# Optimization experiments

Hardware: AMD Instinct MI355X
Metric: run time of the kernel (lower is better)

The kernel has to match this reference:

```python
import jax, jax.numpy as jnp
import numpy as np

IN_F = 512
OUT_F = 512
NOISE_DIM = 128
BATCH = 512
OUT_DIM = IN_F * OUT_F + OUT_F  # 262656
PRIOR_STD = 1.0
PRIOR_SCALE = 1.0
POSTERIOR_SCALE = 1.0


def setup_inputs() -> dict:
    key = jax.random.key(0)
    k1, k2, k3, k4, k5, k6 = jax.random.split(key, 6)
    x = jax.random.normal(k1, (BATCH, IN_F), dtype=jnp.float32)
    prior_x = jax.random.normal(k2, (BATCH, IN_F), dtype=jnp.float32)
    hyper_noise = jax.random.normal(k3, (BATCH, NOISE_DIM), dtype=jnp.float32)
    # hypermodel = nn.Linear(noise_dim, out_dim): kaiming-uniform-ish init approximated by uniform
    bound = 1.0 / np.sqrt(NOISE_DIM)
    hW = jax.random.uniform(k4, (OUT_DIM, NOISE_DIM), jnp.float32, -bound, bound)
    hb = jax.random.uniform(k5, (OUT_DIM,), jnp.float32, -bound, bound)
    # PriorHyperLinear: row-normalized gaussian weight scaled by prior_std (eye), zero bias (prior_mean=0)
    pW = jax.random.normal(k6, (OUT_DIM, NOISE_DIM), dtype=jnp.float32)
    pW = PRIOR_STD * pW / jnp.linalg.norm(pW, axis=1, keepdims=True)
    pb = jnp.zeros((OUT_DIM,), dtype=jnp.float32)
    return {"x": x, "prior_x": prior_x, "hyper_noise": hyper_noise,
            "hW": hW, "hb": hb, "pW": pW, "pb": pb}


def _base_forward(x, params):
    # params: [B, in*out + out] -> per-sample weight [B, in, out], bias [B, out]
    weight = params[:, : IN_F * OUT_F].reshape(-1, IN_F, OUT_F)
    bias = params[:, IN_F * OUT_F:]  # [B, out]
    # bmm(x[:,None,:], weight) + bias -> [B, out]
    return jnp.einsum("bi,bio->bo", x, weight) + bias


def reference(x, prior_x, hyper_noise, hW, hb, pW, pb):
    params = hyper_noise @ hW.T + hb  # [B, out_dim]
    out = _base_forward(x, params)
    prior_params = hyper_noise @ pW.T + pb
    prior_out = _base_forward(prior_x, prior_params)
    return out * POSTERIOR_SCALE + prior_out * PRIOR_SCALE
```

## Files before the change

kernel.cpp:

```cpp
#include <hip/hip_runtime.h>
#include <hip/hip_fp16.h>

#define BATCH 512
#define INF   512
#define OUTF  512
#define ND    128
#define WPART 262144

typedef __attribute__((ext_vector_type(8))) _Float16 half8;
typedef __attribute__((ext_vector_type(2))) _Float16 half2v;
typedef __attribute__((ext_vector_type(4))) float    f32x4;

__device__ inline half8 cvt8(float4 a, float4 b) {
  half2v h0 = __builtin_bit_cast(half2v, __builtin_amdgcn_cvt_pkrtz(a.x, a.y));
  half2v h1 = __builtin_bit_cast(half2v, __builtin_amdgcn_cvt_pkrtz(a.z, a.w));
  half2v h2 = __builtin_bit_cast(half2v, __builtin_amdgcn_cvt_pkrtz(b.x, b.y));
  half2v h3 = __builtin_bit_cast(half2v, __builtin_amdgcn_cvt_pkrtz(b.z, b.w));
  half8 r = { h0[0], h0[1], h1[0], h1[1], h2[0], h2[1], h3[0], h3[1] };
  return r;
}

__global__ void __launch_bounds__(256) transpose_kernel(
    const float* __restrict__ x, const float* __restrict__ px,
    float* __restrict__ xt) {
  __shared__ float t[32][33];
  const float* src = blockIdx.z ? px : x;
  float* dst = xt + ((size_t)blockIdx.z << 18);
  const int bi = blockIdx.x * 32, bb = blockIdx.y * 32;
  const int tx = threadIdx.x & 31, ty = threadIdx.x >> 5;
  #pragma unroll
  for (int r = 0; r < 32; r += 8)
    t[ty + r][tx] = src[(size_t)(bb + ty + r) * 512 + bi + tx];
  __syncthreads();
  #pragma unroll
  for (int r = 0; r < 32; r += 8)
    dst[(size_t)(bi + ty + r) * 512 + bb + tx] = t[tx][ty + r];
}

__global__ void __launch_bounds__(256) tail_kernel(
    const float* __restrict__ hn, const float* __restrict__ hW,
    const float* __restrict__ pW, float* __restrict__ TT) {
  const int bt = blockIdx.x & 7;
  const int bg = blockIdx.x >> 3;
  __shared__ float wsum[64][132];
  __shared__ float hs[32][132];
  {
    int r = threadIdx.x >> 2, seg = threadIdx.x & 3;
    const float4* h4 = (const float4*)(hW + (((size_t)(WPART + bt*64 + r)) << 7) + seg*32);
    const float4* p4 = (const float4*)(pW + (((size_t)(WPART + bt*64 + r)) << 7) + seg*32);
    #pragma unroll
    for (int qq = 0; qq < 8; ++qq) {
      float4 a = h4[qq], b = p4[qq];
      float* d = &wsum[r][seg*32 + qq*4];
      d[0]=a.x+b.x; d[1]=a.y+b.y; d[2]=a.z+b.z; d[3]=a.w+b.w;
    }
    int bb = threadIdx.x >> 3, ch = threadIdx.x & 7;
    const float4* hh = (const float4*)(hn + (((size_t)(bg*32 + bb)) << 7) + ch*16);
    #pragma unroll
    for (int qq = 0; qq < 4; ++qq) {
      float4 a = hh[qq];
      float* d = &hs[bb][ch*16 + qq*4];
      d[0]=a.x; d[1]=a.y; d[2]=a.z; d[3]=a.w;
    }
  }
  __syncthreads();
  const int ol = threadIdx.x & 63, b0 = (threadIdx.x >> 6) * 8;
  float a[8] = {};
  for (int n = 0; n < 128; n += 4) {
    float4 wv = *(const float4*)&wsum[ol][n];
    #pragma unroll
    for (int r = 0; r < 8; ++r) {
      float4 hv = *(const float4*)&hs[b0 + r][n];
      a[r] += hv.x*wv.x + hv.y*wv.y + hv.z*wv.z + hv.w*wv.w;
    }
  }
  #pragma unroll
  for (int r = 0; r < 8; ++r)
    TT[(((size_t)(bg*32 + b0 + r)) << 9) + bt*64 + ol] = a[r];
}

__global__ void __launch_bounds__(1024, 4) gemm_kernel(
    const float* __restrict__ xt, const float* __restrict__ hn,
    const float* __restrict__ hW, const float* __restrict__ pW,
    float* __restrict__ P, int S) {
  const int tid = threadIdx.x;
  const int lane = tid & 63, w = tid >> 6;
  const int l15 = lane & 15, j = lane >> 4;
  const int wrow0 = w << 5;

  const int n0 = blockIdx.x << 6;
  const int q  = blockIdx.y;
  const int spb  = S >> 3;
  const int half = S >> 1;
  const int part = q / half;
  const int rem  = q % half;
  const int nh   = rem / spb;
  const int irange = 512 / spb;
  const int i0   = (rem % spb) * irange;
  const int nst  = irange >> 1;
  const float* srcW = part ? pW : hW;
  const float* xtp  = xt + ((size_t)part << 18);
  const int woff = nh << 5;

  __shared__ half8 ldsW[2][512];
  __shared__ float xr[2][2][512];

  f32x4 acc[2][4] = {};

  const int o_s = tid >> 4;
  const int g_s = tid & 15;
  const int isub_s = g_s >> 3;
  const size_t colbase = (((size_t)(n0 + o_s)) << 7) + woff + ((g_s & 7) << 2);
  const int wdst = (o_s << 7) + (((((g_s >> 1)) ^ (o_s & 7)) << 4) | ((g_s & 1) << 3));

  half8 hnf[2];
  #pragma unroll
  for (int m = 0; m < 2; ++m) {
    int row = wrow0 + m * 16 + l15;
    const float4* hp = (const float4*)(hn + ((size_t)row << 7) + woff + (j << 3));
    hnf[m] = cvt8(hp[0], hp[1]);
  }

  auto loadW = [&](int ph, float4& rw) {
    int i = i0 + 2 * ph + isub_s;
    rw = *(const float4*)(srcW + ((size_t)i << 16) + colbase);
  };
  auto writeW = [&](int buf, float4 rw) {
    unsigned u0 = __builtin_bit_cast(unsigned, __builtin_amdgcn_cvt_pkrtz(rw.x, rw.y));
    unsigned u1 = __builtin_bit_cast(unsigned, __builtin_amdgcn_cvt_pkrtz(rw.z, rw.w));
    uint2 u; u.x = u0; u.y = u1;
    *(uint2*)((char*)&ldsW[buf][0] + wdst) = u;
  };
  auto stageX = [&](int buf, int ph) {
    int i = i0 + 2 * ph + (tid >> 9);
    const float* g = xtp + ((size_t)i << 9) + (tid & 511);
    __builtin_amdgcn_global_load_lds(
        (const __attribute__((address_space(1))) void*)g,
        (__attribute__((address_space(3))) void*)((char*)&xr[buf][0][0] + tid * 4),
        4, 0, 0);
  };
  auto compute = [&](int buf) {
    const char* bW = (const char*)&ldsW[buf][0];
    #pragma unroll
    for (int kk = 0; kk < 2; ++kk) {
      half8 af[2], bf[4];
      #pragma unroll
      for (int m = 0; m < 2; ++m) {
        float xv = xr[buf][kk][wrow0 + m * 16 + l15];
        _Float16 t = (_Float16)xv;
        half8 xb = { t, t, t, t, t, t, t, t };
        af[m] = hnf[m] * xb;
      }
      #pragma unroll
      for (int nn = 0; nn < 4; ++nn) {
        int byte = (((nn << 4) + l15) << 7) + (((((kk << 2) + j)) ^ (l15 & 7)) << 4);
        bf[nn] = *(const half8*)(bW + byte);
      }
      __builtin_amdgcn_s_setprio(1);
      #pragma unroll
      for (int m = 0; m < 2; ++m)
        #pragma unroll
        for (int nn = 0; nn < 4; ++nn)
          acc[m][nn] = __builtin_amdgcn_mfma_f32_16x16x32_f16(
              af[m], bf[nn], acc[m][nn], 0, 0, 0);
      __builtin_amdgcn_s_setprio(0);
    }
  };

  float4 rwA, rwB;
  asm volatile("s_waitcnt vmcnt(0)" ::: "memory");
  loadW(0, rwA);
  stageX(0, 0);
  loadW(1, rwB);
  writeW(0, rwA);

  for (int p = 0; p < nst; p += 2) {
    asm volatile("s_waitcnt vmcnt(1) lgkmcnt(0)" ::: "memory");
    __builtin_amdgcn_s_barrier();
    stageX(1, p + 1);
    if (p + 2 < nst) loadW(p + 2, rwA);
    compute(0);
    writeW(1, rwB);

    if (p + 2 < nst)
      asm volatile("s_waitcnt vmcnt(1) lgkmcnt(0)" ::: "memory");
    else
      asm volatile("s_waitcnt vmcnt(0) lgkmcnt(0)" ::: "memory");
    __builtin_amdgcn_s_barrier();
    if (p + 2 < nst) stageX(0, p + 2);
    if (p + 3 < nst) loadW(p + 3, rwB);
    compute(1);
    if (p + 2 < nst) writeW(0, rwA);
  }

  float* outp = P + ((size_t)q << 18);
  #pragma unroll
  for (int m = 0; m < 2; ++m) {
    int row = wrow0 + m * 16 + (j << 2);
    #pragma unroll
    for (int nn = 0; nn < 4; ++nn) {
      int col = n0 + (nn << 4) + l15;
      float* op = outp + (size_t)row * OUTF + col;
      op[0]    = acc[m][nn][0];
      op[512]  = acc[m][nn][1];
      op[1024] = acc[m][nn][2];
      op[1536] = acc[m][nn][3];
    }
  }
}

__global__ void __launch_bounds__(256) finish_kernel(
    const float* __restrict__ P, const float* __restrict__ x,
    const float* __restrict__ hb, const float* __restrict__ TT,
    float* __restrict__ out, int S) {
  const int o  = blockIdx.x * 256 + threadIdx.x;
  const int b0 = blockIdx.y * 2;
  __shared__ float xs[2][512];
  #pragma unroll
  for (int t = 0; t < 4; ++t) {
    int idx = threadIdx.x + t * 256;
    xs[idx >> 9][idx & 511] = x[((size_t)(b0 + (idx >> 9)) << 9) + (idx & 511)];
  }
  __syncthreads();

  const float bias = hb[WPART + o];
  float a0 = bias, a1 = bias;
  #pragma unroll 16
  for (int i = 0; i < 512; ++i) {
    float hv = hb[(i << 9) + o];
    a0 += xs[0][i] * hv;
    a1 += xs[1][i] * hv;
  }
  a0 += TT[((size_t)b0 << 9) + o];
  a1 += TT[((size_t)(b0 + 1) << 9) + o];

  const float* P0 = P + ((size_t)b0 << 9) + o;
  const float* P1 = P0 + 512;
  float t00 = 0, t01 = 0, t10 = 0, t11 = 0;
  #pragma unroll 4
  for (int k = 0; k < S; k += 2) {
    t00 += P0[(size_t)(k)     << 18];
    t01 += P0[(size_t)(k + 1) << 18];
    t10 += P1[(size_t)(k)     << 18];
    t11 += P1[(size_t)(k + 1) << 18];
  }
  out[((size_t)b0 << 9) + o]       = a0 + t00 + t01;
  out[((size_t)(b0 + 1) << 9) + o] = a1 + t10 + t11;
}

extern "C" void kernel_launch(void* const* d_in, const int* in_sizes, int n_in,
                              void* d_out, int out_size, void* d_ws, size_t ws_size,
                              hipStream_t stream) {
  const float* x  = (const float*)d_in[0];
  const float* px = (const float*)d_in[1];
  const float* hn = (const float*)d_in[2];
  const float* hW = (const float*)d_in[3];
  const float* hb = (const float*)d_in[4];
  const float* pW = (const float*)d_in[5];
  float* out = (float*)d_out;
  float* xt  = (float*)d_ws;
  float* TT  = xt + (1 << 19);
  float* P   = TT + (1 << 18);

  int S = 64;
  while (S > 8 && (((size_t)(3 + S)) << 20) > ws_size) S >>= 1;

  transpose_kernel<<<dim3(16, 16, 2), 256, 0, stream>>>(x, px, xt);
  tail_kernel<<<dim3(128), 256, 0, stream>>>(hn, hW, pW, TT);
  gemm_kernel<<<dim3(8, S), dim3(1024), 0, stream>>>(xt, hn, hW, pW, P, S);
  finish_kernel<<<dim3(2, 256), dim3(256), 0, stream>>>(P, x, hb, TT, out, S);
}
```

Before: 135.2 us.

## Deepen gemm prefetch pipeline, load x directly to registers, halve split count

The gemm kernel no longer stages x into LDS through global_load_lds. Each lane now loads the x scalars it needs straight into registers. The W/x prefetch ring grows from two stages to four register-held stages, and the explicit vmcnt waits are dropped so the compiler inserts them. The split factor S drops from 64 to 32, which doubles the K range per block and reduces partial-sum traffic and finish work, at the cost of fewer blocks and more registers per thread.

```diff
diff --git a/kernel.cpp b/kernel.cpp
--- a/kernel.cpp
+++ b/kernel.cpp
@@ -103,7 +103,6 @@
   const int woff = nh << 5;
 
   __shared__ half8 ldsW[2][512];
-  __shared__ float xr[2][2][512];
 
   f32x4 acc[2][4] = {};
 
@@ -131,26 +130,24 @@
     uint2 u; u.x = u0; u.y = u1;
     *(uint2*)((char*)&ldsW[buf][0] + wdst) = u;
   };
-  auto stageX = [&](int buf, int ph) {
-    int i = i0 + 2 * ph + (tid >> 9);
-    const float* g = xtp + ((size_t)i << 9) + (tid & 511);
-    __builtin_amdgcn_global_load_lds(
-        (const __attribute__((address_space(1))) void*)g,
-        (__attribute__((address_space(3))) void*)((char*)&xr[buf][0][0] + tid * 4),
-        4, 0, 0);
-  };
-  auto compute = [&](int buf) {
+  auto loadX = [&](int ph, float4& xq) {
+    const float* g = xtp + (((size_t)(i0 + 2 * ph)) << 9) + wrow0 + l15;
+    xq.x = g[0];
+    xq.y = g[16];
+    xq.z = g[512];
+    xq.w = g[528];
+  };
+  auto compute = [&](int buf, float4 xq) {
     const char* bW = (const char*)&ldsW[buf][0];
     #pragma unroll
     for (int kk = 0; kk < 2; ++kk) {
       half8 af[2], bf[4];
-      #pragma unroll
-      for (int m = 0; m < 2; ++m) {
-        float xv = xr[buf][kk][wrow0 + m * 16 + l15];
-        _Float16 t = (_Float16)xv;
-        half8 xb = { t, t, t, t, t, t, t, t };
-        af[m] = hnf[m] * xb;
-      }
+      _Float16 t0 = (_Float16)(kk ? xq.z : xq.x);
+      _Float16 t1 = (_Float16)(kk ? xq.w : xq.y);
+      half8 xb0 = { t0, t0, t0, t0, t0, t0, t0, t0 };
+      half8 xb1 = { t1, t1, t1, t1, t1, t1, t1, t1 };
+      af[0] = hnf[0] * xb0;
+      af[1] = hnf[1] * xb1;
       #pragma unroll
       for (int nn = 0; nn < 4; ++nn) {
         int byte = (((nn << 4) + l15) << 7) + (((((kk << 2) + j)) ^ (l15 & 7)) << 4);
@@ -167,31 +164,30 @@
     }
   };
 
-  float4 rwA, rwB;
-  asm volatile("s_waitcnt vmcnt(0)" ::: "memory");
-  loadW(0, rwA);
-  stageX(0, 0);
-  loadW(1, rwB);
-  writeW(0, rwA);
-
-  for (int p = 0; p < nst; p += 2) {
-    asm volatile("s_waitcnt vmcnt(1) lgkmcnt(0)" ::: "memory");
-    __builtin_amdgcn_s_barrier();
-    stageX(1, p + 1);
-    if (p + 2 < nst) loadW(p + 2, rwA);
-    compute(0);
-    writeW(1, rwB);
-
-    if (p + 2 < nst)
-      asm volatile("s_waitcnt vmcnt(1) lgkmcnt(0)" ::: "memory");
-    else
-      asm volatile("s_waitcnt vmcnt(0) lgkmcnt(0)" ::: "memory");
-    __builtin_amdgcn_s_barrier();
-    if (p + 2 < nst) stageX(0, p + 2);
-    if (p + 3 < nst) loadW(p + 3, rwB);
-    compute(1);
-    if (p + 2 < nst) writeW(0, rwA);
-  }
+  float4 rw0, rw1, rw2, rw3, xq0, xq1, xq2, xq3;
+  loadW(0, rw0); loadX(0, xq0);
+  loadW(1, rw1); loadX(1, xq1);
+  loadW(2, rw2); loadX(2, xq2);
+  loadW(3, rw3); loadX(3, xq3);
+  writeW(0, rw0);
+
+#define PHASE(p, RWCUR, XQCUR, RWNEXT, BUF)                                \
+  {                                                                        \
+    asm volatile("s_waitcnt lgkmcnt(0)" ::: "memory");                     \
+    __builtin_amdgcn_s_barrier();                                          \
+    if ((p) + 4 < nst) loadW((p) + 4, RWCUR);                              \
+    compute(BUF, XQCUR);                                                   \
+    if ((p) + 4 < nst) loadX((p) + 4, XQCUR);                              \
+    if ((p) + 1 < nst) writeW(BUF ^ 1, RWNEXT);                            \
+  }
+
+  for (int p = 0; p < nst; p += 4) {
+    PHASE(p + 0, rw0, xq0, rw1, 0)
+    PHASE(p + 1, rw1, xq1, rw2, 1)
+    PHASE(p + 2, rw2, xq2, rw3, 0)
+    PHASE(p + 3, rw3, xq3, rw0, 1)
+  }
+#undef PHASE
 
   float* outp = P + ((size_t)q << 18);
   #pragma unroll
@@ -262,7 +258,7 @@
   float* TT  = xt + (1 << 19);
   float* P   = TT + (1 << 18);
 
-  int S = 64;
+  int S = 32;
   while (S > 8 && (((size_t)(3 + S)) << 20) > ws_size) S >>= 1;
 
   transpose_kernel<<<dim3(16, 16, 2), 256, 0, stream>>>(x, px, xt);
```

Result: faster. 116.3 us (-14.0%).
